# Kernel tuning notes

Hardware: AMD Instinct MI355X
Metric: run time of the kernel (lower is better)

The kernel has to match this reference:

```python
import jax, jax.numpy as jnp
import numpy as np

EPS = 1e-6

def _rmsnorm(x, w):
    # normalize over last (head_dim) axis
    return x * jax.lax.rsqrt(jnp.mean(x * x, axis=-1, keepdims=True) + EPS) * w

def _rope(x, cos, sin):
    # x: [B, H, S, D]; cos/sin: [S, D]
    d = x.shape[-1]
    x1, x2 = x[..., : d // 2], x[..., d // 2 :]
    rot = jnp.concatenate([-x2, x1], axis=-1)
    return x * cos[None, None] + rot * sin[None, None]

def setup_inputs() -> dict:
    key = jax.random.key(0)
    B, S, D_MODEL = 1, 2048, 2048
    HEADS, HEAD_DIM, NKV = 32, 64, 8
    d_out = HEADS * HEAD_DIM
    kv_d_out = NKV * HEAD_DIM
    ks = jax.random.split(key, 8)
    x = jax.random.normal(ks[0], (B, S, D_MODEL), dtype=jnp.float32)
    # RoPE tables
    inv_freq = 1.0 / (10000.0 ** (jnp.arange(0, HEAD_DIM, 2, dtype=jnp.float32) / HEAD_DIM))
    pos = jnp.arange(S, dtype=jnp.float32)
    ang = pos[:, None] * inv_freq[None, :]            # [S, D/2]
    ang = jnp.concatenate([ang, ang], axis=-1)        # [S, D]
    sin, cos = jnp.sin(ang), jnp.cos(ang)
    mask = jnp.tril(jnp.ones((S, S), dtype=bool))     # causal: True = attend
    sd = 0.02
    Wq = jax.random.normal(ks[1], (D_MODEL, d_out), dtype=jnp.float32) * sd
    Wk = jax.random.normal(ks[2], (D_MODEL, kv_d_out), dtype=jnp.float32) * sd
    Wv = jax.random.normal(ks[3], (D_MODEL, kv_d_out), dtype=jnp.float32) * sd
    Wo = jax.random.normal(ks[4], (d_out, D_MODEL), dtype=jnp.float32) * sd
    bo = jnp.zeros((D_MODEL,), dtype=jnp.float32)
    q_scale = jnp.ones((HEAD_DIM,), dtype=jnp.float32)
    k_scale = jnp.ones((HEAD_DIM,), dtype=jnp.float32)
    return {"x": x, "sin": sin, "cos": cos, "mask": mask, "Wq": Wq, "Wk": Wk,
            "Wv": Wv, "Wo": Wo, "bo": bo, "q_scale": q_scale, "k_scale": k_scale}

def reference(x, sin, cos, mask, Wq, Wk, Wv, Wo, bo, q_scale, k_scale):
    B, S, _ = x.shape
    HEADS, HEAD_DIM, NKV = 32, 64, 8
    GS = HEADS // NKV  # group size = 4
    q = (x @ Wq).reshape(B, S, HEADS, HEAD_DIM).transpose(0, 2, 1, 3)  # [B,H,S,D]
    k = (x @ Wk).reshape(B, S, NKV, HEAD_DIM).transpose(0, 2, 1, 3)    # [B,G,S,D]
    v = (x @ Wv).reshape(B, S, NKV, HEAD_DIM).transpose(0, 2, 1, 3)    # [B,G,S,D]
    q = _rmsnorm(q, q_scale)
    k = _rmsnorm(k, k_scale)
    q = _rope(q, cos, sin)
    k = _rope(k, cos, sin)
    # GQA without materializing repeated k/v: group query heads per kv group
    qg = q.reshape(B, NKV, GS, S, HEAD_DIM)
    scale = 1.0 / jnp.sqrt(jnp.asarray(HEAD_DIM, dtype=x.dtype))
    scores = jnp.einsum('bghqd,bgkd->bghqk', qg, k) * scale  # [B,G,Gs,S,S]
    scores = jnp.where(mask[None, None, None], scores, jnp.asarray(-jnp.inf, dtype=scores.dtype))
    attn = jax.nn.softmax(scores, axis=-1)
    out = jnp.einsum('bghqk,bgkd->bghqd', attn, v)            # [B,G,Gs,S,D]
    out = out.reshape(B, HEADS, S, HEAD_DIM).transpose(0, 2, 1, 3).reshape(B, S, HEADS * HEAD_DIM)
    return out @ Wo + bo
```

## Files before the change

kernel.cpp:

```cpp
#include <hip/hip_runtime.h>
#include <stdint.h>


typedef __bf16 bf16x8 __attribute__((ext_vector_type(8)));
typedef __bf16 bf16x4v __attribute__((ext_vector_type(4)));
typedef float f32x4 __attribute__((ext_vector_type(4)));

#define MFMA_BF16(a, b, c) __builtin_amdgcn_mfma_f32_16x16x32_bf16(a, b, c, 0, 0, 0)

#if __has_builtin(__builtin_amdgcn_exp2f)
#define EXP2F(x) __builtin_amdgcn_exp2f(x)
#else
#define EXP2F(x) __expf((x) * 0.69314718055994531f)
#endif

#define QSCALE 0.18033688011112042f
#define SHIFT2 11.541560327111707f

__device__ __forceinline__ unsigned short f2bf(float f) {
  unsigned int u = __float_as_uint(f);
  u += 0x7fffu + ((u >> 16) & 1u);
  return (unsigned short)(u >> 16);
}
__device__ __forceinline__ float bf2f(unsigned short b) {
  return __uint_as_float(((unsigned int)b) << 16);
}

__device__ __forceinline__ void gload_lds16(const unsigned short* gsrc,
                                            unsigned short* ldst) {
  __builtin_amdgcn_global_load_lds(
      (const __attribute__((address_space(1))) unsigned int*)gsrc,
      (__attribute__((address_space(3))) unsigned int*)ldst, 16, 0, 0);
}

__global__ __launch_bounds__(256) void cvt_bf16(const float* __restrict__ X,
                                                unsigned short* __restrict__ Y, int n) {
  int i = (blockIdx.x * 256 + threadIdx.x) * 4;
  if (i < n) {
    float4 v = *(const float4*)&X[i];
    ushort4 o;
    o.x = f2bf(v.x); o.y = f2bf(v.y); o.z = f2bf(v.z); o.w = f2bf(v.w);
    *(ushort4*)&Y[i] = o;
  }
}

__global__ __launch_bounds__(256) void transpose_all(const float* __restrict__ Wq,
                                                     const float* __restrict__ Wk,
                                                     const float* __restrict__ Wv,
                                                     const float* __restrict__ Wo,
                                                     unsigned short* __restrict__ Wqkvt,
                                                     unsigned short* __restrict__ Wot) {
  int bx = blockIdx.x;
  const float* W;
  unsigned short* T;
  int N, nb;
  if (bx < 32)      { W = Wq; T = Wqkvt;                     N = 2048; nb = bx * 64; }
  else if (bx < 40) { W = Wk; T = Wqkvt + 2048 * 2048;       N = 512;  nb = (bx - 32) * 64; }
  else if (bx < 48) { W = Wv; T = Wqkvt + (size_t)2560 * 2048; N = 512; nb = (bx - 40) * 64; }
  else              { W = Wo; T = Wot;                       N = 2048; nb = (bx - 48) * 64; }
  int kb = blockIdx.y * 64;
  int tid = threadIdx.x;
  __shared__ float tile[64][65];
#pragma unroll
  for (int i = 0; i < 16; i++) {
    int idx = tid + i * 256;
    int r = idx >> 6, c = idx & 63;
    tile[r][c] = W[(size_t)(kb + r) * N + nb + c];
  }
  __syncthreads();
#pragma unroll
  for (int i = 0; i < 8; i++) {
    int idx = tid + i * 256;
    int r = idx >> 5, cp = idx & 31;
    ushort2 o;
    o.x = f2bf(tile[2 * cp][r]);
    o.y = f2bf(tile[2 * cp + 1][r]);
    *(ushort2*)&T[(size_t)(nb + r) * 2048 + kb + 2 * cp] = o;
  }
}

#define GEMM_CORE2(A_, B_, m0_, n0_, K_)                                       \
  int quad = lane >> 4, l16 = lane & 15;                                       \
  int rsub = lane >> 3, csub = lane & 7;                                       \
  int chunk = csub ^ rsub;                                                     \
  const unsigned short* gA = &A_[(size_t)(m0_ + w * 32 + rsub) * K_ + chunk * 8]; \
  const unsigned short* gB = &B_[(size_t)(n0_ + w * 64 + rsub) * K_ + chunk * 8]; \
  unsigned short* lA = As + (w * 32) * 64 + lane * 8;                          \
  unsigned short* lB = Bs + (w * 64) * 64 + lane * 8;                          \
  int slotL = quad ^ (l16 & 7);                                                \
  f32x4 acc[4][4];                                                             \
  _Pragma("unroll") for (int i = 0; i < 4; i++)                                \
      _Pragma("unroll") for (int j = 0; j < 4; j++)                            \
          acc[i][j] = (f32x4){0.f, 0.f, 0.f, 0.f};                             \
  for (int k0 = 0; k0 < K_; k0 += 64) {                                        \
    __syncthreads();                                                           \
    _Pragma("unroll") for (int c = 0; c < 4; c++)                              \
        gload_lds16(gA + (size_t)c * 8 * K_ + k0, lA + c * 8 * 64);            \
    _Pragma("unroll") for (int c = 0; c < 8; c++)                              \
        gload_lds16(gB + (size_t)c * 8 * K_ + k0, lB + c * 8 * 64);            \
    __syncthreads();                                                           \
    bf16x8 af[4][2], bfr[4][2];                                                \
    _Pragma("unroll") for (int i = 0; i < 4; i++) {                            \
      int base = (i * 16 + l16) * 64;                                          \
      af[i][0] = *(const bf16x8*)&As[base + slotL * 8];                        \
      af[i][1] = *(const bf16x8*)&As[base + (slotL ^ 4) * 8];                  \
    }                                                                          \
    _Pragma("unroll") for (int j = 0; j < 4; j++) {                            \
      int base = (w * 64 + j * 16 + l16) * 64;                                 \
      bfr[j][0] = *(const bf16x8*)&Bs[base + slotL * 8];                       \
      bfr[j][1] = *(const bf16x8*)&Bs[base + (slotL ^ 4) * 8];                 \
    }                                                                          \
    _Pragma("unroll") for (int kc = 0; kc < 2; kc++)                           \
        _Pragma("unroll") for (int i = 0; i < 4; i++)                          \
            _Pragma("unroll") for (int j = 0; j < 4; j++)                      \
                acc[i][j] = MFMA_BF16(af[i][kc], bfr[j][kc], acc[i][j]);       \
  }

__global__ __launch_bounds__(128, 3) void gemm_qkv(const unsigned short* __restrict__ A,
                                                   const unsigned short* __restrict__ B,
                                                   const float* __restrict__ sinp,
                                                   const float* __restrict__ cosp,
                                                   const float* __restrict__ q_scale,
                                                   const float* __restrict__ k_scale,
                                                   unsigned short* __restrict__ qh,
                                                   unsigned short* __restrict__ kh,
                                                   unsigned short* __restrict__ vtmp) {
  __shared__ __align__(16) unsigned short As[64 * 64];
  __shared__ __align__(16) unsigned short Bs[128 * 64];
  int tid = threadIdx.x;
  int w = tid >> 6, lane = tid & 63;
  int m0 = blockIdx.y * 64;
  int n0 = blockIdx.x * 128;
  GEMM_CORE2(A, B, m0, n0, 2048)

  int hd = blockIdx.x * 2 + w;
  if (hd < 40) {
    const float* scl = (hd < 32) ? q_scale : k_scale;
    float wsc[4];
#pragma unroll
    for (int j = 0; j < 4; j++) wsc[j] = scl[j * 16 + l16];
    float oscale = (hd < 32) ? QSCALE : 1.0f;
#pragma unroll
    for (int i = 0; i < 4; i++)
#pragma unroll
      for (int r = 0; r < 4; r++) {
        float ss = 0.f;
#pragma unroll
        for (int j = 0; j < 4; j++) ss += acc[i][j][r] * acc[i][j][r];
#pragma unroll
        for (int off = 8; off; off >>= 1) ss += __shfl_xor(ss, off);
        float inv = rsqrtf(ss * (1.f / 64.f) + 1e-6f);
        int s = m0 + i * 16 + quad * 4 + r;
        float xn[4];
#pragma unroll
        for (int j = 0; j < 4; j++) xn[j] = acc[i][j][r] * inv * wsc[j];
#pragma unroll
        for (int j = 0; j < 4; j++) {
          int d = j * 16 + l16;
          float rot = (j < 2) ? -xn[j + 2] : xn[j - 2];
          float out = (xn[j] * cosp[s * 64 + d] + rot * sinp[s * 64 + d]) * oscale;
          if (hd < 32) qh[(size_t)s * 2048 + hd * 64 + d] = f2bf(out);
          else         kh[(size_t)s * 512 + (hd - 32) * 64 + d] = f2bf(out);
        }
      }
  } else {
    int g = hd - 40;
#pragma unroll
    for (int i = 0; i < 4; i++)
#pragma unroll
      for (int r = 0; r < 4; r++) {
        int s = m0 + i * 16 + quad * 4 + r;
#pragma unroll
        for (int j = 0; j < 4; j++)
          vtmp[(size_t)s * 512 + g * 64 + j * 16 + l16] = f2bf(acc[i][j][r]);
      }
  }
}

__global__ __launch_bounds__(128, 3) void gemm_out(const unsigned short* __restrict__ A,
                                                   const unsigned short* __restrict__ B,
                                                   float* __restrict__ C,
                                                   const float* __restrict__ bias) {
  __shared__ __align__(16) unsigned short As[64 * 64];
  __shared__ __align__(16) unsigned short Bs[128 * 64];
  int tid = threadIdx.x;
  int w = tid >> 6, lane = tid & 63;
  int m0 = blockIdx.y * 64;
  int n0 = blockIdx.x * 128;
  GEMM_CORE2(A, B, m0, n0, 2048)

#pragma unroll
  for (int i = 0; i < 4; i++) {
    int row = m0 + i * 16 + quad * 4;
#pragma unroll
    for (int j = 0; j < 4; j++) {
      int col = n0 + w * 64 + j * 16 + l16;
      float b = bias[col];
#pragma unroll
      for (int r = 0; r < 4; r++)
        C[(size_t)(row + r) * 2048 + col] = acc[i][j][r] + b;
    }
  }
}

__global__ __launch_bounds__(256) void v_transpose(const unsigned short* __restrict__ vtmp,
                                                   unsigned short* __restrict__ vt) {
  __shared__ unsigned short tile[64][65];
  int s0 = blockIdx.x * 64;
  int g = blockIdx.y;
  int tid = threadIdx.x;
#pragma unroll
  for (int i = 0; i < 16; i++) {
    int idx = tid + i * 256;
    int r = idx >> 6, c = idx & 63;
    tile[r][c] = vtmp[(size_t)(s0 + r) * 512 + g * 64 + c];
  }
  __syncthreads();
#pragma unroll
  for (int i = 0; i < 16; i++) {
    int idx = tid + i * 256;
    int d = idx >> 6, slot = idx & 63;
    int key = (slot & 3) * 16 + (slot >> 2);
    vt[(size_t)(g * 64 + d) * 2048 + s0 + slot] = tile[key][d];
  }
}

__global__ __launch_bounds__(256, 4) void attention(const unsigned short* __restrict__ qh,
                                                    const unsigned short* __restrict__ kh,
                                                    const unsigned short* __restrict__ vt,
                                                    unsigned short* __restrict__ Opart,
                                                    float* __restrict__ Lpart) {
  int h = blockIdx.y;
  int g = h >> 2;
  int z = blockIdx.z;
  int tile = (blockIdx.x + blockIdx.y) & 31;
  int q0 = tile * 64;
  int w = threadIdx.x >> 6;
  int lane = threadIdx.x & 63;
  int quad = lane >> 4;
  int l16 = lane & 15;
  int qrow0 = q0 + w * 16;

  __shared__ __align__(16) unsigned short Ks[64 * 64];
  __shared__ __align__(16) unsigned short Vs[64 * 64];
  __shared__ __align__(16) unsigned short Plds[4][16 * 72];
  unsigned short* P = &Plds[w][0];

  int rsub = lane >> 3;
  int csub = lane & 7;
  int chunk = csub ^ rsub;

  const unsigned short* kg0 = &kh[(size_t)(w * 16 + rsub) * 512 + g * 64 + chunk * 8];
  const unsigned short* kg1 = kg0 + 8 * 512;
  const unsigned short* vg0 = &vt[(size_t)(g * 64 + w * 16 + rsub) * 2048 + chunk * 8];
  const unsigned short* vg1 = vg0 + 8 * 2048;
  unsigned short* kl0 = &Ks[(w * 16) * 64] + lane * 8;
  unsigned short* kl1 = kl0 + 8 * 64;
  unsigned short* vl0 = &Vs[(w * 16) * 64] + lane * 8;
  unsigned short* vl1 = vl0 + 8 * 64;

  int posL = quad ^ (l16 & 7);
  int fL = l16 * 64 + posL * 8;
  int fH = l16 * 64 + (posL ^ 4) * 8;

  bf16x8 aq0 = *(const bf16x8*)&qh[(size_t)(qrow0 + l16) * 2048 + h * 64 + quad * 8];
  bf16x8 aq1 = *(const bf16x8*)&qh[(size_t)(qrow0 + l16) * 2048 + h * 64 + 32 + quad * 8];

  f32x4 o[4];
#pragma unroll
  for (int j = 0; j < 4; j++) o[j] = (f32x4){0.f, 0.f, 0.f, 0.f};
  float l_run[4] = {0.f, 0.f, 0.f, 0.f};

  int T = tile + 1;
  int it0 = z ? (T >> 1) : 0;
  int it1 = z ? T : (T >> 1);
  for (int it = it0; it < it1; ++it) {
    int n0 = it << 6;
    __syncthreads();
    gload_lds16(kg0 + (size_t)n0 * 512, kl0);
    gload_lds16(kg1 + (size_t)n0 * 512, kl1);
    gload_lds16(vg0 + n0, vl0);
    gload_lds16(vg1 + n0, vl1);
    __syncthreads();

    f32x4 s[4];
#pragma unroll
    for (int t = 0; t < 4; ++t) {
      bf16x8 kfl = *(const bf16x8*)&Ks[t * 1024 + fL];
      bf16x8 kfh = *(const bf16x8*)&Ks[t * 1024 + fH];
      f32x4 zz = (f32x4){0.f, 0.f, 0.f, 0.f};
      zz = MFMA_BF16(aq0, kfl, zz);
      s[t] = MFMA_BF16(aq1, kfh, zz);
    }

    float pv[4][4];
    if (it == T - 1) {
#pragma unroll
      for (int t = 0; t < 4; ++t) {
        int key = n0 + t * 16 + l16;
#pragma unroll
        for (int r = 0; r < 4; ++r) {
          int row = qrow0 + quad * 4 + r;
          float p = (key <= row) ? EXP2F(s[t][r] - SHIFT2) : 0.f;
          l_run[r] += p;
          pv[t][r] = p;
        }
      }
    } else {
#pragma unroll
      for (int t = 0; t < 4; ++t)
#pragma unroll
        for (int r = 0; r < 4; ++r) {
          float p = EXP2F(s[t][r] - SHIFT2);
          l_run[r] += p;
          pv[t][r] = p;
        }
    }
#pragma unroll
    for (int r = 0; r < 4; ++r) {
      bf16x4v pk;
      pk[0] = (__bf16)pv[0][r]; pk[1] = (__bf16)pv[1][r];
      pk[2] = (__bf16)pv[2][r]; pk[3] = (__bf16)pv[3][r];
      *(bf16x4v*)&P[(quad * 4 + r) * 72 + l16 * 4] = pk;
    }
    __threadfence_block();
    bf16x8 pf0 = *(const bf16x8*)&P[l16 * 72 + quad * 8];
    bf16x8 pf1 = *(const bf16x8*)&P[l16 * 72 + 32 + quad * 8];

#pragma unroll
    for (int j = 0; j < 4; ++j) {
      bf16x8 vfl = *(const bf16x8*)&Vs[j * 1024 + fL];
      bf16x8 vfh = *(const bf16x8*)&Vs[j * 1024 + fH];
      o[j] = MFMA_BF16(pf0, vfl, o[j]);
      o[j] = MFMA_BF16(pf1, vfh, o[j]);
    }
  }

#pragma unroll
  for (int r = 0; r < 4; r++) {
    float sum = l_run[r];
#pragma unroll
    for (int off = 8; off; off >>= 1) sum += __shfl_xor(sum, off);
    if (l16 == 0)
      Lpart[(size_t)z * 65536 + (qrow0 + quad * 4 + r) * 32 + h] = sum;
  }
#pragma unroll
  for (int j = 0; j < 4; j++)
#pragma unroll
    for (int r = 0; r < 4; r++)
      Opart[((size_t)z * 2048 + qrow0 + quad * 4 + r) * 2048 + h * 64 + j * 16 + l16] =
          f2bf(o[j][r]);
}

__global__ __launch_bounds__(256) void combine(const unsigned short* __restrict__ Opart,
                                               const float* __restrict__ Lpart,
                                               unsigned short* __restrict__ aout) {
  int idx = blockIdx.x * 256 + threadIdx.x;
  int s = idx >> 9;
  int col = (idx & 511) * 4;
  int h = col >> 6;
  float l = Lpart[s * 32 + h] + Lpart[65536 + s * 32 + h];
  float linv = 1.f / l;
  ushort4 a = *(const ushort4*)&Opart[(size_t)s * 2048 + col];
  ushort4 b = *(const ushort4*)&Opart[(size_t)(2048 + s) * 2048 + col];
  ushort4 o;
  o.x = f2bf((bf2f(a.x) + bf2f(b.x)) * linv);
  o.y = f2bf((bf2f(a.y) + bf2f(b.y)) * linv);
  o.z = f2bf((bf2f(a.z) + bf2f(b.z)) * linv);
  o.w = f2bf((bf2f(a.w) + bf2f(b.w)) * linv);
  *(ushort4*)&aout[(size_t)s * 2048 + col] = o;
}

extern "C" void kernel_launch(void* const* d_in, const int* in_sizes, int n_in,
                              void* d_out, int out_size, void* d_ws, size_t ws_size,
                              hipStream_t stream) {
  (void)in_sizes; (void)n_in; (void)out_size; (void)ws_size;
  const float* x    = (const float*)d_in[0];
  const float* sinp = (const float*)d_in[1];
  const float* cosp = (const float*)d_in[2];
  const float* Wq = (const float*)d_in[4];
  const float* Wk = (const float*)d_in[5];
  const float* Wv = (const float*)d_in[6];
  const float* Wo = (const float*)d_in[7];
  const float* bo = (const float*)d_in[8];
  const float* q_scale = (const float*)d_in[9];
  const float* k_scale = (const float*)d_in[10];
  float* outp = (float*)d_out;

  uint8_t* ws = (uint8_t*)d_ws;
  const size_t MB = 1024 * 1024;
  unsigned short* xb    = (unsigned short*)(ws);
  unsigned short* Wqkvt = (unsigned short*)(ws + 8 * MB);
  unsigned short* Wot   = (unsigned short*)(ws + 20 * MB);
  unsigned short* qh    = (unsigned short*)(ws + 28 * MB);
  unsigned short* kh    = (unsigned short*)(ws + 36 * MB);
  unsigned short* vtmp  = (unsigned short*)(ws + 38 * MB);
  unsigned short* vt    = (unsigned short*)(ws + 40 * MB);
  unsigned short* aout  = (unsigned short*)(ws + 42 * MB);
  unsigned short* Opart = (unsigned short*)(ws + 50 * MB);
  float*          Lpart = (float*)(ws + 66 * MB);

  cvt_bf16<<<4096, 256, 0, stream>>>(x, xb, 2048 * 2048);
  transpose_all<<<dim3(80, 32), 256, 0, stream>>>(Wq, Wk, Wv, Wo, Wqkvt, Wot);
  gemm_qkv<<<dim3(24, 32), 128, 0, stream>>>(xb, Wqkvt, sinp, cosp, q_scale, k_scale,
                                             qh, kh, vtmp);
  v_transpose<<<dim3(32, 8), 256, 0, stream>>>(vtmp, vt);
  attention<<<dim3(32, 32, 2), 256, 0, stream>>>(qh, kh, vt, Opart, Lpart);
  combine<<<4096, 256, 0, stream>>>(Opart, Lpart, aout);
  gemm_out<<<dim3(16, 32), 128, 0, stream>>>(aout, Wot, outp, bo);
}
```

Measured before the change: 238.7 us.

## Double-buffer LDS staging in GEMMs and attention, widen GEMM blocks to four waves

Both GEMM kernels now ping-pong between two LDS stages, prefetching the next K-slice while MFMAs run on the current one. They also move from 2 to 4 waves per block (a 2x2 wave grid with 32x64 sub-tiles each). The attention kernel applies the same two-stage K/V prefetch, so each loop iteration needs one barrier instead of two. The aim is to hide global-to-LDS latency behind compute, at the cost of more LDS per block and a correctness dependence on the async LDS loads being complete at the barrier.

```diff
diff --git a/kernel.cpp b/kernel.cpp
--- a/kernel.cpp
+++ b/kernel.cpp
@@ -54,10 +54,10 @@
   const float* W;
   unsigned short* T;
   int N, nb;
-  if (bx < 32)      { W = Wq; T = Wqkvt;                     N = 2048; nb = bx * 64; }
-  else if (bx < 40) { W = Wk; T = Wqkvt + 2048 * 2048;       N = 512;  nb = (bx - 32) * 64; }
-  else if (bx < 48) { W = Wv; T = Wqkvt + (size_t)2560 * 2048; N = 512; nb = (bx - 40) * 64; }
-  else              { W = Wo; T = Wot;                       N = 2048; nb = (bx - 48) * 64; }
+  if (bx < 32)      { W = Wq; T = Wqkvt;                       N = 2048; nb = bx * 64; }
+  else if (bx < 40) { W = Wk; T = Wqkvt + 2048 * 2048;         N = 512;  nb = (bx - 32) * 64; }
+  else if (bx < 48) { W = Wv; T = Wqkvt + (size_t)2560 * 2048; N = 512;  nb = (bx - 40) * 64; }
+  else              { W = Wo; T = Wot;                         N = 2048; nb = (bx - 48) * 64; }
   int kb = blockIdx.y * 64;
   int tid = threadIdx.x;
   __shared__ float tile[64][65];
@@ -79,44 +79,62 @@
   }
 }
 
-#define GEMM_CORE2(A_, B_, m0_, n0_, K_)                                       \
+#define GEMM_DBUF(A_, B_, m0_, n0_)                                            \
   int quad = lane >> 4, l16 = lane & 15;                                       \
+  int wrow = (w & 1) * 32, wcol = (w >> 1) * 64;                               \
   int rsub = lane >> 3, csub = lane & 7;                                       \
   int chunk = csub ^ rsub;                                                     \
-  const unsigned short* gA = &A_[(size_t)(m0_ + w * 32 + rsub) * K_ + chunk * 8]; \
-  const unsigned short* gB = &B_[(size_t)(n0_ + w * 64 + rsub) * K_ + chunk * 8]; \
-  unsigned short* lA = As + (w * 32) * 64 + lane * 8;                          \
-  unsigned short* lB = Bs + (w * 64) * 64 + lane * 8;                          \
   int slotL = quad ^ (l16 & 7);                                                \
-  f32x4 acc[4][4];                                                             \
-  _Pragma("unroll") for (int i = 0; i < 4; i++)                                \
+  const unsigned short* gA = &A_[(size_t)(m0_ + w * 16 + rsub) * 2048 + chunk * 8]; \
+  const unsigned short* gB = &B_[(size_t)(n0_ + w * 32 + rsub) * 2048 + chunk * 8]; \
+  int laOff = (w * 16) * 64 + lane * 8;                                        \
+  int lbOff = 64 * 64 + (w * 32) * 64 + lane * 8;                              \
+  f32x4 acc[2][4];                                                             \
+  _Pragma("unroll") for (int i = 0; i < 2; i++)                                \
       _Pragma("unroll") for (int j = 0; j < 4; j++)                            \
           acc[i][j] = (f32x4){0.f, 0.f, 0.f, 0.f};                             \
-  for (int k0 = 0; k0 < K_; k0 += 64) {                                        \
+  {                                                                            \
+    unsigned short* sp = &Stage[0][0];                                         \
+    gload_lds16(gA, sp + laOff);                                               \
+    gload_lds16(gA + 8 * 2048, sp + laOff + 8 * 64);                           \
+    gload_lds16(gB, sp + lbOff);                                               \
+    gload_lds16(gB + 8 * 2048, sp + lbOff + 8 * 64);                           \
+    gload_lds16(gB + 16 * 2048, sp + lbOff + 16 * 64);                         \
+    gload_lds16(gB + 24 * 2048, sp + lbOff + 24 * 64);                         \
+  }                                                                            \
+  for (int k0 = 0; k0 < 2048; k0 += 64) {                                      \
     __syncthreads();                                                           \
-    _Pragma("unroll") for (int c = 0; c < 4; c++)                              \
-        gload_lds16(gA + (size_t)c * 8 * K_ + k0, lA + c * 8 * 64);            \
-    _Pragma("unroll") for (int c = 0; c < 8; c++)                              \
-        gload_lds16(gB + (size_t)c * 8 * K_ + k0, lB + c * 8 * 64);            \
-    __syncthreads();                                                           \
-    bf16x8 af[4][2], bfr[4][2];                                                \
-    _Pragma("unroll") for (int i = 0; i < 4; i++) {                            \
-      int base = (i * 16 + l16) * 64;                                          \
+    unsigned short* cur = &Stage[(k0 >> 6) & 1][0];                            \
+    unsigned short* nxt = &Stage[((k0 >> 6) + 1) & 1][0];                      \
+    if (k0 + 64 < 2048) {                                                      \
+      int kn = k0 + 64;                                                        \
+      gload_lds16(gA + kn, nxt + laOff);                                       \
+      gload_lds16(gA + 8 * 2048 + kn, nxt + laOff + 8 * 64);                   \
+      gload_lds16(gB + kn, nxt + lbOff);                                       \
+      gload_lds16(gB + 8 * 2048 + kn, nxt + lbOff + 8 * 64);                   \
+      gload_lds16(gB + 16 * 2048 + kn, nxt + lbOff + 16 * 64);                 \
+      gload_lds16(gB + 24 * 2048 + kn, nxt + lbOff + 24 * 64);                 \
+    }                                                                          \
+    const unsigned short* As = cur;                                            \
+    const unsigned short* Bs = cur + 64 * 64;                                  \
+    bf16x8 af[2][2], bfr[4][2];                                                \
+    _Pragma("unroll") for (int i = 0; i < 2; i++) {                            \
+      int base = (wrow + i * 16 + l16) * 64;                                   \
       af[i][0] = *(const bf16x8*)&As[base + slotL * 8];                        \
       af[i][1] = *(const bf16x8*)&As[base + (slotL ^ 4) * 8];                  \
     }                                                                          \
     _Pragma("unroll") for (int j = 0; j < 4; j++) {                            \
-      int base = (w * 64 + j * 16 + l16) * 64;                                 \
+      int base = (wcol + j * 16 + l16) * 64;                                   \
       bfr[j][0] = *(const bf16x8*)&Bs[base + slotL * 8];                       \
       bfr[j][1] = *(const bf16x8*)&Bs[base + (slotL ^ 4) * 8];                 \
     }                                                                          \
     _Pragma("unroll") for (int kc = 0; kc < 2; kc++)                           \
-        _Pragma("unroll") for (int i = 0; i < 4; i++)                          \
+        _Pragma("unroll") for (int i = 0; i < 2; i++)                          \
             _Pragma("unroll") for (int j = 0; j < 4; j++)                      \
                 acc[i][j] = MFMA_BF16(af[i][kc], bfr[j][kc], acc[i][j]);       \
   }
 
-__global__ __launch_bounds__(128, 3) void gemm_qkv(const unsigned short* __restrict__ A,
+__global__ __launch_bounds__(256, 3) void gemm_qkv(const unsigned short* __restrict__ A,
                                                    const unsigned short* __restrict__ B,
                                                    const float* __restrict__ sinp,
                                                    const float* __restrict__ cosp,
@@ -125,15 +143,14 @@
                                                    unsigned short* __restrict__ qh,
                                                    unsigned short* __restrict__ kh,
                                                    unsigned short* __restrict__ vtmp) {
-  __shared__ __align__(16) unsigned short As[64 * 64];
-  __shared__ __align__(16) unsigned short Bs[128 * 64];
+  __shared__ __align__(16) unsigned short Stage[2][192 * 64];
   int tid = threadIdx.x;
   int w = tid >> 6, lane = tid & 63;
   int m0 = blockIdx.y * 64;
   int n0 = blockIdx.x * 128;
-  GEMM_CORE2(A, B, m0, n0, 2048)
-
-  int hd = blockIdx.x * 2 + w;
+  GEMM_DBUF(A, B, m0, n0)
+
+  int hd = blockIdx.x * 2 + (w >> 1);
   if (hd < 40) {
     const float* scl = (hd < 32) ? q_scale : k_scale;
     float wsc[4];
@@ -141,7 +158,7 @@
     for (int j = 0; j < 4; j++) wsc[j] = scl[j * 16 + l16];
     float oscale = (hd < 32) ? QSCALE : 1.0f;
 #pragma unroll
-    for (int i = 0; i < 4; i++)
+    for (int i = 0; i < 2; i++)
 #pragma unroll
       for (int r = 0; r < 4; r++) {
         float ss = 0.f;
@@ -150,7 +167,7 @@
 #pragma unroll
         for (int off = 8; off; off >>= 1) ss += __shfl_xor(ss, off);
         float inv = rsqrtf(ss * (1.f / 64.f) + 1e-6f);
-        int s = m0 + i * 16 + quad * 4 + r;
+        int s = m0 + wrow + i * 16 + quad * 4 + r;
         float xn[4];
 #pragma unroll
         for (int j = 0; j < 4; j++) xn[j] = acc[i][j][r] * inv * wsc[j];
@@ -166,10 +183,10 @@
   } else {
     int g = hd - 40;
 #pragma unroll
-    for (int i = 0; i < 4; i++)
+    for (int i = 0; i < 2; i++)
 #pragma unroll
       for (int r = 0; r < 4; r++) {
-        int s = m0 + i * 16 + quad * 4 + r;
+        int s = m0 + wrow + i * 16 + quad * 4 + r;
 #pragma unroll
         for (int j = 0; j < 4; j++)
           vtmp[(size_t)s * 512 + g * 64 + j * 16 + l16] = f2bf(acc[i][j][r]);
@@ -177,24 +194,23 @@
   }
 }
 
-__global__ __launch_bounds__(128, 3) void gemm_out(const unsigned short* __restrict__ A,
+__global__ __launch_bounds__(256, 3) void gemm_out(const unsigned short* __restrict__ A,
                                                    const unsigned short* __restrict__ B,
                                                    float* __restrict__ C,
                                                    const float* __restrict__ bias) {
-  __shared__ __align__(16) unsigned short As[64 * 64];
-  __shared__ __align__(16) unsigned short Bs[128 * 64];
+  __shared__ __align__(16) unsigned short Stage[2][192 * 64];
   int tid = threadIdx.x;
   int w = tid >> 6, lane = tid & 63;
   int m0 = blockIdx.y * 64;
   int n0 = blockIdx.x * 128;
-  GEMM_CORE2(A, B, m0, n0, 2048)
-
-#pragma unroll
-  for (int i = 0; i < 4; i++) {
-    int row = m0 + i * 16 + quad * 4;
+  GEMM_DBUF(A, B, m0, n0)
+
+#pragma unroll
+  for (int i = 0; i < 2; i++) {
+    int row = m0 + wrow + i * 16 + quad * 4;
 #pragma unroll
     for (int j = 0; j < 4; j++) {
-      int col = n0 + w * 64 + j * 16 + l16;
+      int col = n0 + wcol + j * 16 + l16;
       float b = bias[col];
 #pragma unroll
       for (int r = 0; r < 4; r++)
@@ -241,8 +257,7 @@
   int l16 = lane & 15;
   int qrow0 = q0 + w * 16;
 
-  __shared__ __align__(16) unsigned short Ks[64 * 64];
-  __shared__ __align__(16) unsigned short Vs[64 * 64];
+  __shared__ __align__(16) unsigned short Stage[2][8192];
   __shared__ __align__(16) unsigned short Plds[4][16 * 72];
   unsigned short* P = &Plds[w][0];
 
@@ -250,14 +265,10 @@
   int csub = lane & 7;
   int chunk = csub ^ rsub;
 
-  const unsigned short* kg0 = &kh[(size_t)(w * 16 + rsub) * 512 + g * 64 + chunk * 8];
-  const unsigned short* kg1 = kg0 + 8 * 512;
-  const unsigned short* vg0 = &vt[(size_t)(g * 64 + w * 16 + rsub) * 2048 + chunk * 8];
-  const unsigned short* vg1 = vg0 + 8 * 2048;
-  unsigned short* kl0 = &Ks[(w * 16) * 64] + lane * 8;
-  unsigned short* kl1 = kl0 + 8 * 64;
-  unsigned short* vl0 = &Vs[(w * 16) * 64] + lane * 8;
-  unsigned short* vl1 = vl0 + 8 * 64;
+  const unsigned short* kg = &kh[(size_t)(w * 16 + rsub) * 512 + g * 64 + chunk * 8];
+  const unsigned short* vg = &vt[(size_t)(g * 64 + w * 16 + rsub) * 2048 + chunk * 8];
+  int klOff = (w * 16) * 64 + lane * 8;
+  int vlOff = 4096 + (w * 16) * 64 + lane * 8;
 
   int posL = quad ^ (l16 & 7);
   int fL = l16 * 64 + posL * 8;
@@ -274,14 +285,28 @@
   int T = tile + 1;
   int it0 = z ? (T >> 1) : 0;
   int it1 = z ? T : (T >> 1);
+  if (it0 < it1) {
+    unsigned short* sp = &Stage[0][0];
+    int n0 = it0 << 6;
+    gload_lds16(kg + (size_t)n0 * 512, sp + klOff);
+    gload_lds16(kg + (size_t)(n0 + 8) * 512, sp + klOff + 8 * 64);
+    gload_lds16(vg + n0, sp + vlOff);
+    gload_lds16(vg + n0 + 8 * 2048, sp + vlOff + 8 * 64);
+  }
   for (int it = it0; it < it1; ++it) {
+    __syncthreads();
+    const unsigned short* cur = &Stage[(it - it0) & 1][0];
+    unsigned short* nxt = &Stage[(it - it0 + 1) & 1][0];
+    if (it + 1 < it1) {
+      int nn = (it + 1) << 6;
+      gload_lds16(kg + (size_t)nn * 512, nxt + klOff);
+      gload_lds16(kg + (size_t)(nn + 8) * 512, nxt + klOff + 8 * 64);
+      gload_lds16(vg + nn, nxt + vlOff);
+      gload_lds16(vg + nn + 8 * 2048, nxt + vlOff + 8 * 64);
+    }
     int n0 = it << 6;
-    __syncthreads();
-    gload_lds16(kg0 + (size_t)n0 * 512, kl0);
-    gload_lds16(kg1 + (size_t)n0 * 512, kl1);
-    gload_lds16(vg0 + n0, vl0);
-    gload_lds16(vg1 + n0, vl1);
-    __syncthreads();
+    const unsigned short* Ks = cur;
+    const unsigned short* Vs = cur + 4096;
 
     f32x4 s[4];
 #pragma unroll
@@ -402,10 +427,10 @@
 
   cvt_bf16<<<4096, 256, 0, stream>>>(x, xb, 2048 * 2048);
   transpose_all<<<dim3(80, 32), 256, 0, stream>>>(Wq, Wk, Wv, Wo, Wqkvt, Wot);
-  gemm_qkv<<<dim3(24, 32), 128, 0, stream>>>(xb, Wqkvt, sinp, cosp, q_scale, k_scale,
+  gemm_qkv<<<dim3(24, 32), 256, 0, stream>>>(xb, Wqkvt, sinp, cosp, q_scale, k_scale,
                                              qh, kh, vtmp);
   v_transpose<<<dim3(32, 8), 256, 0, stream>>>(vtmp, vt);
   attention<<<dim3(32, 32, 2), 256, 0, stream>>>(qh, kh, vt, Opart, Lpart);
   combine<<<4096, 256, 0, stream>>>(Opart, Lpart, aout);
-  gemm_out<<<dim3(16, 32), 128, 0, stream>>>(aout, Wot, outp, bo);
-}
+  gemm_out<<<dim3(16, 32), 256, 0, stream>>>(aout, Wot, outp, bo);
+}
```

Measured after the change: 236.3 us. Within noise of the previous version (-1.0%).
